# Performance work log

Measured on AMD Instinct MI355X. Metric: run time of the kernel, lower is better.

The kernel has to match this reference:

```python
import jax, jax.numpy as jnp
import numpy as np

# tiny-cuda-nn HashGrid config from the module
N_LEVELS = 12
F_PER_LEVEL = 2
LOG2_T = 16
T = 1 << LOG2_T            # 65536 entries per level
BASE_RES = 4
PER_LEVEL_SCALE = 1.61
HASH_PRIME_Y = np.uint32(2654435761)
HIDDEN = 256
OUT = 3
N_POINTS = 1048576

# per-level scale / resolution (tcnn: scale = base*s^l - 1, res = ceil(scale)+1)
_LEVEL_SCALES = [BASE_RES * (PER_LEVEL_SCALE ** l) - 1.0 for l in range(N_LEVELS)]
_LEVEL_RES = [int(np.ceil(s)) + 1 for s in _LEVEL_SCALES]

_CORNERS = np.array([[0, 0], [1, 0], [0, 1], [1, 1]], dtype=np.uint32)  # [4,2]


def hash_encode(x, tables):
    """x: [N,2] in [0,1); tables: [L,T,F]. Returns [N, L*F]."""
    offs_u = jnp.asarray(_CORNERS)                      # [4,2] uint32
    offs_f = offs_u.astype(x.dtype)                     # [4,2]
    feats = []
    for l in range(N_LEVELS):
        s = _LEVEL_SCALES[l]
        res = _LEVEL_RES[l]
        pos = x * jnp.asarray(s, x.dtype) + 0.5         # [N,2]
        p0f = jnp.floor(pos)
        w = pos - p0f                                   # [N,2] frac, differentiable
        p0 = p0f.astype(jnp.uint32)                     # [N,2]
        c = p0[:, None, :] + offs_u[None]               # [N,4,2] corner coords
        # bilinear weight per corner: prod over dims of (w if offset==1 else 1-w)
        wc = jnp.where(offs_f[None] == 1.0, w[:, None, :], 1.0 - w[:, None, :]).prod(-1)  # [N,4]
        if res * res <= T:
            # dense (tight grid) indexing
            cx = jnp.minimum(c[..., 0], np.uint32(res - 1))
            cy = jnp.minimum(c[..., 1], np.uint32(res - 1))
            idx = cx + cy * np.uint32(res)
        else:
            # spatial hash: x*1 XOR y*prime, masked to table size
            idx = (c[..., 0] ^ (c[..., 1] * HASH_PRIME_Y)) & np.uint32(T - 1)
        f = tables[l][idx.astype(jnp.int32)]            # [N,4,F] gather
        feats.append((wc[..., None] * f).sum(axis=1))   # [N,F]
    return jnp.concatenate(feats, axis=-1)              # [N, L*F]


def setup_inputs() -> dict:
    key = jax.random.key(0)
    ks = jax.random.split(key, 10)
    x = jax.random.uniform(ks[0], (N_POINTS, 2), dtype=jnp.float32)
    # tcnn initializes hash tables uniform in [-1e-4, 1e-4]
    tables = jax.random.uniform(ks[1], (N_LEVELS, T, F_PER_LEVEL), dtype=jnp.float32,
                                minval=-1e-4, maxval=1e-4)
    d_in = N_LEVELS * F_PER_LEVEL

    def lin(k, fan_in, fan_out):
        bound = 1.0 / np.sqrt(fan_in)
        kw, kb = jax.random.split(k)
        W = jax.random.uniform(kw, (fan_in, fan_out), dtype=jnp.float32, minval=-bound, maxval=bound)
        b = jax.random.uniform(kb, (fan_out,), dtype=jnp.float32, minval=-bound, maxval=bound)
        return W, b

    W1, b1 = lin(ks[2], d_in, HIDDEN)
    W2, b2 = lin(ks[3], HIDDEN, HIDDEN)
    W3, b3 = lin(ks[4], HIDDEN, HIDDEN)
    Wo, bo = lin(ks[5], HIDDEN, OUT)
    return {"x": x, "tables": tables, "W1": W1, "b1": b1, "W2": W2, "b2": b2,
            "W3": W3, "b3": b3, "Wo": Wo, "bo": bo}


def reference(x, tables, W1, b1, W2, b2, W3, b3, Wo, bo):
    enc = hash_encode(x, tables)                        # [N,24]
    h = jax.nn.relu(enc @ W1 + b1)
    h = jax.nn.relu(h @ W2 + b2)
    h = jax.nn.relu(h @ W3 + b3)
    return h @ Wo + bo                                  # [N,3]
```

## Files before the change

kernel.cpp:

```cpp
#include <hip/hip_runtime.h>

typedef _Float16 f16;
typedef _Float16 f16x2 __attribute__((ext_vector_type(2)));
typedef _Float16 f16x4 __attribute__((ext_vector_type(4)));
typedef _Float16 f16x8 __attribute__((ext_vector_type(8)));
typedef float    f32x4 __attribute__((ext_vector_type(4)));

#define ES 40
#define NPTS 256

static __device__ const float c_scale[12] = {
  3.0f, 5.44f, 9.3684f, 15.693124f, 25.87592964f, 42.2702467204f,
  68.665097219844f, 111.16080652394884f, 179.5788985035576f,
  289.7320265907278f, 467.0785628110717f, 752.6064861258255f };
static __device__ const unsigned c_res[12] = {4,7,11,17,27,44,70,113,181,291,469,754};

__global__ __launch_bounds__(256) void prep_weights(
    const float* __restrict__ W1, const float* __restrict__ W2,
    const float* __restrict__ W3, const float* __restrict__ Wo,
    f16* __restrict__ ws)
{
  int i = blockIdx.x * 256 + threadIdx.x;
  if (i < 8192) {
    int o = i >> 5, k = i & 31;
    ws[i] = (k < 24) ? (f16)W1[k * 256 + o] : (f16)0.0f;
  } else if (i < 73728) {
    int j = i - 8192; int o = j >> 8, k = j & 255;
    ws[i] = (f16)W2[k * 256 + o];
  } else if (i < 139264) {
    int j = i - 73728; int o = j >> 8, k = j & 255;
    ws[i] = (f16)W3[k * 256 + o];
  } else if (i < 143360) {
    int j = i - 139264; int o = j >> 8, k = j & 255;
    ws[i] = (o < 3) ? (f16)Wo[k * 3 + o] : (f16)0.0f;
  }
}

__device__ __forceinline__ f16x2 enc_level_dense(
    float2 xy, float s, unsigned res, const float* __restrict__ tbl)
{
  float px = __fadd_rn(__fmul_rn(xy.x, s), 0.5f);
  float py = __fadd_rn(__fmul_rn(xy.y, s), 0.5f);
  float fx = floorf(px), fy = floorf(py);
  float wx = px - fx, wy = py - fy;
  unsigned ix = (unsigned)fx, iy = (unsigned)fy;
  unsigned rm = res - 1u;
  unsigned x0 = min(ix, rm);
  unsigned y0 = min(iy, rm), y1 = min(iy + 1u, rm);
  bool xe = (ix >= rm);
  f32x4 r0 = *(const f32x4*)(tbl + (x0 + y0 * res) * 2);
  f32x4 r1 = *(const f32x4*)(tbl + (x0 + y1 * res) * 2);
  float f00x = r0[0], f00y = r0[1];
  float f10x = xe ? r0[0] : r0[2], f10y = xe ? r0[1] : r0[3];
  float f01x = r1[0], f01y = r1[1];
  float f11x = xe ? r1[0] : r1[2], f11y = xe ? r1[1] : r1[3];
  float w00 = (1.f - wx) * (1.f - wy), w10 = wx * (1.f - wy);
  float w01 = (1.f - wx) * wy,         w11 = wx * wy;
  float e0 = w00 * f00x + w10 * f10x + w01 * f01x + w11 * f11x;
  float e1 = w00 * f00y + w10 * f10y + w01 * f01y + w11 * f11y;
  f16x2 pk; pk[0] = (f16)e0; pk[1] = (f16)e1;
  return pk;
}

__device__ __forceinline__ f16x2 enc_level_hash(
    float2 xy, float s, const float* __restrict__ tbl)
{
  float px = __fadd_rn(__fmul_rn(xy.x, s), 0.5f);
  float py = __fadd_rn(__fmul_rn(xy.y, s), 0.5f);
  float fx = floorf(px), fy = floorf(py);
  float wx = px - fx, wy = py - fy;
  unsigned ix = (unsigned)fx, iy = (unsigned)fy;
  unsigned h0 = iy * 2654435761u, h1 = (iy + 1u) * 2654435761u;
  unsigned i00 = (ix ^ h0) & 65535u,  i10 = ((ix + 1u) ^ h0) & 65535u;
  unsigned i01 = (ix ^ h1) & 65535u,  i11 = ((ix + 1u) ^ h1) & 65535u;
  const float2* tb = (const float2*)tbl;
  float2 f00 = tb[i00], f10 = tb[i10], f01 = tb[i01], f11 = tb[i11];
  float w00 = (1.f - wx) * (1.f - wy), w10 = wx * (1.f - wy);
  float w01 = (1.f - wx) * wy,         w11 = wx * wy;
  float e0 = w00 * f00.x + w10 * f10.x + w01 * f01.x + w11 * f11.x;
  float e1 = w00 * f00.y + w10 * f10.y + w01 * f01.y + w11 * f11.y;
  f16x2 pk; pk[0] = (f16)e0; pk[1] = (f16)e1;
  return pk;
}

template<bool NEXT_OUT>
__device__ __forceinline__ void layer256_pipe(
    f16* __restrict__ h, const f16* __restrict__ WT,
    const f32x4* bv, f16x8* cur0, f16x8* cur1,
    const f16* __restrict__ WTn, const float* __restrict__ bn,
    f16x8* nxt0, f16x8* nxt1, f32x4* bvn, f16x8* aout,
    const int* vbase, const int* wbase, int w, int l15, int g)
{
  f32x4 acc[2][16];
  #pragma unroll
  for (int mt = 0; mt < 2; ++mt)
    #pragma unroll
    for (int nt = 0; nt < 16; ++nt) acc[mt][nt] = bv[mt];

  f16x8 abuf[3][2];
  #pragma unroll
  for (int mt = 0; mt < 2; ++mt) { abuf[0][mt] = cur0[mt]; abuf[1][mt] = cur1[mt]; }

  const char* hb = (const char*)h;
  #pragma unroll
  for (int ks = 0; ks < 8; ++ks) {
    if (ks < 6) {
      #pragma unroll
      for (int mt = 0; mt < 2; ++mt)
        abuf[(ks+2)%3][mt] = *(const f16x8*)(WT + (w*32 + mt*16 + l15)*256 + (ks+2)*32 + g*8);
    } else if (ks == 6) {
      if (NEXT_OUT) {
        #pragma unroll
        for (int q = 0; q < 4; ++q)
          aout[q] = *(const f16x8*)(WTn + l15*256 + q*32 + g*8);
      } else {
        #pragma unroll
        for (int mt = 0; mt < 2; ++mt)
          nxt0[mt] = *(const f16x8*)(WTn + (w*32 + mt*16 + l15)*256 + g*8);
        #pragma unroll
        for (int mt = 0; mt < 2; ++mt)
          bvn[mt] = *(const f32x4*)(bn + w*32 + mt*16 + g*4);
      }
    } else {
      if (NEXT_OUT) {
        #pragma unroll
        for (int q = 0; q < 4; ++q)
          aout[4+q] = *(const f16x8*)(WTn + l15*256 + (4+q)*32 + g*8);
      } else {
        #pragma unroll
        for (int mt = 0; mt < 2; ++mt)
          nxt1[mt] = *(const f16x8*)(WTn + (w*32 + mt*16 + l15)*256 + 32 + g*8);
      }
    }
    #pragma unroll
    for (int nt = 0; nt < 16; ++nt) {
      f16x8 b = *(const f16x8*)(hb + vbase[ks] + nt*8192);
      #pragma unroll
      for (int mt = 0; mt < 2; ++mt)
        acc[mt][nt] = __builtin_amdgcn_mfma_f32_16x16x32_f16(abuf[ks%3][mt], b, acc[mt][nt], 0, 0, 0);
    }
  }
  __syncthreads();
  #pragma unroll
  for (int mt = 0; mt < 2; ++mt) {
    #pragma unroll
    for (int nt = 0; nt < 16; ++nt) {
      f16x4 hv;
      #pragma unroll
      for (int r = 0; r < 4; ++r) {
        float v = acc[mt][nt][r];
        hv[r] = (f16)fmaxf(v, 0.0f);
      }
      *(f16x4*)((char*)h + wbase[mt] + nt*8192) = hv;
    }
  }
  __syncthreads();
}

__global__ __launch_bounds__(512, 2) void hashmlp_kernel(
    const float* __restrict__ x, const float* __restrict__ tables,
    const float* __restrict__ b1, const float* __restrict__ b2,
    const float* __restrict__ b3, const float* __restrict__ bo,
    const f16* __restrict__ ws, float* __restrict__ out)
{
  __shared__ __align__(16) f16 s_enc[NPTS * ES];
  __shared__ __align__(16) f16 s_h[NPTS * 256];

  const int tid = threadIdx.x;
  const int blk = blockIdx.x;
  const int w = tid >> 6, lane = tid & 63;
  const int l15 = lane & 15, g = lane >> 4;

  const f16* W1T = ws;
  const f16* W2T = ws + 8192;
  const f16* W3T = ws + 73728;
  const f16* WoT = ws + 139264;

  f16x8 a1[2], pn0[2], pn1[2];
  f32x4 bvA[2], bvB[2];
  #pragma unroll
  for (int mt = 0; mt < 2; ++mt) {
    a1[mt]  = *(const f16x8*)(W1T + (w*32 + mt*16 + l15)*32 + g*8);
    pn0[mt] = *(const f16x8*)(W2T + (w*32 + mt*16 + l15)*256 + g*8);
    pn1[mt] = *(const f16x8*)(W2T + (w*32 + mt*16 + l15)*256 + 32 + g*8);
    bvA[mt] = *(const f32x4*)(b1 + w*32 + mt*16 + g*4);
    bvB[mt] = *(const f32x4*)(b2 + w*32 + mt*16 + g*4);
  }
  float bo0 = bo[0], bo1 = bo[1], bo2 = bo[2];

  int vbase[8], wbase[2];
  {
    int K = (l15 & 7) << 4;
    #pragma unroll
    for (int ks = 0; ks < 8; ++ks)
      vbase[ks] = l15*512 + ((ks*64 + g*16) ^ K);
    #pragma unroll
    for (int mt = 0; mt < 2; ++mt)
      wbase[mt] = l15*512 + (((w*32 + mt*16 + g*4)*2) ^ K);
  }

  {
    int p = tid >> 1, sub = tid & 1;
    int gp = blk * NPTS + p;
    float2 xy = ((const float2*)x)[gp];
    #pragma unroll
    for (int j = 0; j < 5; ++j) {
      int l = j * 2 + sub;
      f16x2 pk = enc_level_dense(xy, c_scale[l], c_res[l], tables + l * 131072);
      *(f16x2*)(&s_enc[p * ES + l * 2]) = pk;
    }
    {
      int l = 10 + sub;
      f16x2 pk = enc_level_hash(xy, c_scale[l], tables + l * 131072);
      *(f16x2*)(&s_enc[p * ES + l * 2]) = pk;
    }
    f16x4 z; z[0] = (f16)0.0f; z[1] = (f16)0.0f; z[2] = (f16)0.0f; z[3] = (f16)0.0f;
    *(f16x4*)(&s_enc[p * ES + 24 + sub * 4]) = z;
  }
  __syncthreads();

  {
    f32x4 acc[2][16];
    #pragma unroll
    for (int mt = 0; mt < 2; ++mt)
      #pragma unroll
      for (int nt = 0; nt < 16; ++nt) acc[mt][nt] = bvA[mt];
    #pragma unroll
    for (int nt = 0; nt < 16; ++nt) {
      f16x8 b = *(const f16x8*)(&s_enc[(nt*16 + l15) * ES + g*8]);
      #pragma unroll
      for (int mt = 0; mt < 2; ++mt)
        acc[mt][nt] = __builtin_amdgcn_mfma_f32_16x16x32_f16(a1[mt], b, acc[mt][nt], 0, 0, 0);
    }
    #pragma unroll
    for (int mt = 0; mt < 2; ++mt) {
      #pragma unroll
      for (int nt = 0; nt < 16; ++nt) {
        f16x4 hv;
        #pragma unroll
        for (int r = 0; r < 4; ++r) {
          float v = acc[mt][nt][r];
          hv[r] = (f16)fmaxf(v, 0.0f);
        }
        *(f16x4*)((char*)s_h + wbase[mt] + nt*8192) = hv;
      }
    }
  }
  __syncthreads();

  f16x8 qn0[2], qn1[2], aout[8];
  f32x4 bvC[2];
  layer256_pipe<false>(s_h, W2T, bvB, pn0, pn1, W3T, b3, qn0, qn1, bvC, aout,
                       vbase, wbase, w, l15, g);
  layer256_pipe<true >(s_h, W3T, bvC, qn0, qn1, WoT, nullptr, pn0, pn1, bvC, aout,
                       vbase, wbase, w, l15, g);

  {
    f32x4 acc0 = (f32x4)0.0f, acc1 = (f32x4)0.0f;
    const char* hb = (const char*)s_h;
    #pragma unroll
    for (int ks = 0; ks < 8; ++ks) {
      f16x8 b0 = *(const f16x8*)(hb + vbase[ks] + (2*w+0)*8192);
      f16x8 b1v = *(const f16x8*)(hb + vbase[ks] + (2*w+1)*8192);
      acc0 = __builtin_amdgcn_mfma_f32_16x16x32_f16(aout[ks], b0, acc0, 0, 0, 0);
      acc1 = __builtin_amdgcn_mfma_f32_16x16x32_f16(aout[ks], b1v, acc1, 0, 0, 0);
    }
    if (g == 0) {
      int gp0 = blk * NPTS + (2*w+0) * 16 + l15;
      int gp1 = blk * NPTS + (2*w+1) * 16 + l15;
      out[gp0 * 3 + 0] = acc0[0] + bo0;
      out[gp0 * 3 + 1] = acc0[1] + bo1;
      out[gp0 * 3 + 2] = acc0[2] + bo2;
      out[gp1 * 3 + 0] = acc1[0] + bo0;
      out[gp1 * 3 + 1] = acc1[1] + bo1;
      out[gp1 * 3 + 2] = acc1[2] + bo2;
    }
  }
}

extern "C" void kernel_launch(void* const* d_in, const int* in_sizes, int n_in,
                              void* d_out, int out_size, void* d_ws, size_t ws_size,
                              hipStream_t stream) {
  const float* x  = (const float*)d_in[0];
  const float* tb = (const float*)d_in[1];
  const float* W1 = (const float*)d_in[2];
  const float* b1 = (const float*)d_in[3];
  const float* W2 = (const float*)d_in[4];
  const float* b2 = (const float*)d_in[5];
  const float* W3 = (const float*)d_in[6];
  const float* b3 = (const float*)d_in[7];
  const float* Wo = (const float*)d_in[8];
  const float* bo = (const float*)d_in[9];
  f16* ws = (f16*)d_ws;

  prep_weights<<<560, 256, 0, stream>>>(W1, W2, W3, Wo, ws);
  hashmlp_kernel<<<4096, 512, 0, stream>>>(x, tb, b1, b2, b3, bo, ws, (float*)d_out);
}
```

Measured before the change: 363.8 us.

## Switch MLP layers to 32x32x16 MFMA tiles with 128-point, 4-wave blocks

Replaces the 16x16x32 MFMA tiling of the hidden layers with 32x32x16 MFMA, giving each wave 64 output neurons by 128 points. The block shrinks from 256 points and 8 waves to 128 points and 4 waves, and the grid doubles. The larger MFMA tile is meant to raise operand reuse per LDS read and cut the number of LDS B-fragment loads. In exchange it uses more accumulator registers per wave, adds more weight fragment loads per wave, and needs new swizzled address tables; the encoding step and the output layer keep their previous structure.

```diff
diff --git a/kernel.cpp b/kernel.cpp
--- a/kernel.cpp
+++ b/kernel.cpp
@@ -4,10 +4,11 @@
 typedef _Float16 f16x2 __attribute__((ext_vector_type(2)));
 typedef _Float16 f16x4 __attribute__((ext_vector_type(4)));
 typedef _Float16 f16x8 __attribute__((ext_vector_type(8)));
-typedef float    f32x4 __attribute__((ext_vector_type(4)));
+typedef float    f32x4  __attribute__((ext_vector_type(4)));
+typedef float    f32x16 __attribute__((ext_vector_type(16)));
 
 #define ES 40
-#define NPTS 256
+#define NPTS 128
 
 static __device__ const float c_scale[12] = {
   3.0f, 5.44f, 9.3684f, 15.693124f, 25.87592964f, 42.2702467204f,
@@ -84,18 +85,26 @@
 }
 
 template<bool NEXT_OUT>
-__device__ __forceinline__ void layer256_pipe(
+__device__ __forceinline__ void layer256_32(
     f16* __restrict__ h, const f16* __restrict__ WT,
-    const f32x4* bv, f16x8* cur0, f16x8* cur1,
+    const f32x4 (&bv)[2][4], f16x8* cur0, f16x8* cur1,
     const f16* __restrict__ WTn, const float* __restrict__ bn,
-    f16x8* nxt0, f16x8* nxt1, f32x4* bvn, f16x8* aout,
-    const int* vbase, const int* wbase, int w, int l15, int g)
-{
-  f32x4 acc[2][16];
+    f16x8* nxt0, f16x8* nxt1, f32x4 (*bvn)[4], f16x8* aout,
+    const int* vbase, const int (&wb)[2][4],
+    int w, int l31, int g2, int l15, int g)
+{
+  f32x16 acc[2][4];
   #pragma unroll
   for (int mt = 0; mt < 2; ++mt)
     #pragma unroll
-    for (int nt = 0; nt < 16; ++nt) acc[mt][nt] = bv[mt];
+    for (int rq = 0; rq < 4; ++rq) {
+      f32x4 t = bv[mt][rq];
+      #pragma unroll
+      for (int nt = 0; nt < 4; ++nt)
+        #pragma unroll
+        for (int j = 0; j < 4; ++j)
+          acc[mt][nt][rq*4+j] = t[j];
+    }
 
   f16x8 abuf[3][2];
   #pragma unroll
@@ -103,12 +112,12 @@
 
   const char* hb = (const char*)h;
   #pragma unroll
-  for (int ks = 0; ks < 8; ++ks) {
-    if (ks < 6) {
+  for (int ks = 0; ks < 16; ++ks) {
+    if (ks < 14) {
       #pragma unroll
       for (int mt = 0; mt < 2; ++mt)
-        abuf[(ks+2)%3][mt] = *(const f16x8*)(WT + (w*32 + mt*16 + l15)*256 + (ks+2)*32 + g*8);
-    } else if (ks == 6) {
+        abuf[(ks+2)%3][mt] = *(const f16x8*)(WT + (w*64 + mt*32 + l31)*256 + (ks+2)*16 + g2*8);
+    } else if (ks == 14) {
       if (NEXT_OUT) {
         #pragma unroll
         for (int q = 0; q < 4; ++q)
@@ -116,10 +125,12 @@
       } else {
         #pragma unroll
         for (int mt = 0; mt < 2; ++mt)
-          nxt0[mt] = *(const f16x8*)(WTn + (w*32 + mt*16 + l15)*256 + g*8);
+          nxt0[mt] = *(const f16x8*)(WTn + (w*64 + mt*32 + l31)*256 + g2*8);
         #pragma unroll
         for (int mt = 0; mt < 2; ++mt)
-          bvn[mt] = *(const f32x4*)(bn + w*32 + mt*16 + g*4);
+          #pragma unroll
+          for (int rq = 0; rq < 4; ++rq)
+            bvn[mt][rq] = *(const f32x4*)(bn + w*64 + mt*32 + rq*8 + g2*4);
       }
     } else {
       if (NEXT_OUT) {
@@ -129,35 +140,34 @@
       } else {
         #pragma unroll
         for (int mt = 0; mt < 2; ++mt)
-          nxt1[mt] = *(const f16x8*)(WTn + (w*32 + mt*16 + l15)*256 + 32 + g*8);
-      }
-    }
-    #pragma unroll
-    for (int nt = 0; nt < 16; ++nt) {
-      f16x8 b = *(const f16x8*)(hb + vbase[ks] + nt*8192);
+          nxt1[mt] = *(const f16x8*)(WTn + (w*64 + mt*32 + l31)*256 + 16 + g2*8);
+      }
+    }
+    #pragma unroll
+    for (int nt = 0; nt < 4; ++nt) {
+      f16x8 b = *(const f16x8*)(hb + vbase[ks] + nt*16384);
       #pragma unroll
       for (int mt = 0; mt < 2; ++mt)
-        acc[mt][nt] = __builtin_amdgcn_mfma_f32_16x16x32_f16(abuf[ks%3][mt], b, acc[mt][nt], 0, 0, 0);
+        acc[mt][nt] = __builtin_amdgcn_mfma_f32_32x32x16_f16(abuf[ks%3][mt], b, acc[mt][nt], 0, 0, 0);
     }
   }
   __syncthreads();
   #pragma unroll
-  for (int mt = 0; mt < 2; ++mt) {
-    #pragma unroll
-    for (int nt = 0; nt < 16; ++nt) {
-      f16x4 hv;
-      #pragma unroll
-      for (int r = 0; r < 4; ++r) {
-        float v = acc[mt][nt][r];
-        hv[r] = (f16)fmaxf(v, 0.0f);
-      }
-      *(f16x4*)((char*)h + wbase[mt] + nt*8192) = hv;
-    }
-  }
+  for (int mt = 0; mt < 2; ++mt)
+    #pragma unroll
+    for (int nt = 0; nt < 4; ++nt)
+      #pragma unroll
+      for (int rq = 0; rq < 4; ++rq) {
+        f16x4 hv;
+        #pragma unroll
+        for (int j = 0; j < 4; ++j)
+          hv[j] = (f16)fmaxf(acc[mt][nt][rq*4+j], 0.0f);
+        *(f16x4*)((char*)h + wb[mt][rq] + nt*16384) = hv;
+      }
   __syncthreads();
 }
 
-__global__ __launch_bounds__(512, 2) void hashmlp_kernel(
+__global__ __launch_bounds__(256, 2) void hashmlp_kernel(
     const float* __restrict__ x, const float* __restrict__ tables,
     const float* __restrict__ b1, const float* __restrict__ b2,
     const float* __restrict__ b3, const float* __restrict__ bo,
@@ -169,6 +179,7 @@
   const int tid = threadIdx.x;
   const int blk = blockIdx.x;
   const int w = tid >> 6, lane = tid & 63;
+  const int l31 = lane & 31, g2 = lane >> 5;
   const int l15 = lane & 15, g = lane >> 4;
 
   const f16* W1T = ws;
@@ -176,27 +187,35 @@
   const f16* W3T = ws + 73728;
   const f16* WoT = ws + 139264;
 
-  f16x8 a1[2], pn0[2], pn1[2];
-  f32x4 bvA[2], bvB[2];
+  f16x8 a1[2][2], pn0[2], pn1[2];
+  f32x4 bvA[2][4], bvB[2][4];
   #pragma unroll
   for (int mt = 0; mt < 2; ++mt) {
-    a1[mt]  = *(const f16x8*)(W1T + (w*32 + mt*16 + l15)*32 + g*8);
-    pn0[mt] = *(const f16x8*)(W2T + (w*32 + mt*16 + l15)*256 + g*8);
-    pn1[mt] = *(const f16x8*)(W2T + (w*32 + mt*16 + l15)*256 + 32 + g*8);
-    bvA[mt] = *(const f32x4*)(b1 + w*32 + mt*16 + g*4);
-    bvB[mt] = *(const f32x4*)(b2 + w*32 + mt*16 + g*4);
+    #pragma unroll
+    for (int ks = 0; ks < 2; ++ks)
+      a1[ks][mt] = *(const f16x8*)(W1T + (w*64 + mt*32 + l31)*32 + ks*16 + g2*8);
+    pn0[mt] = *(const f16x8*)(W2T + (w*64 + mt*32 + l31)*256 + g2*8);
+    pn1[mt] = *(const f16x8*)(W2T + (w*64 + mt*32 + l31)*256 + 16 + g2*8);
+    #pragma unroll
+    for (int rq = 0; rq < 4; ++rq) {
+      bvA[mt][rq] = *(const f32x4*)(b1 + w*64 + mt*32 + rq*8 + g2*4);
+      bvB[mt][rq] = *(const f32x4*)(b2 + w*64 + mt*32 + rq*8 + g2*4);
+    }
   }
   float bo0 = bo[0], bo1 = bo[1], bo2 = bo[2];
 
-  int vbase[8], wbase[2];
+  int vbase[16];
+  int wb[2][4];
   {
-    int K = (l15 & 7) << 4;
-    #pragma unroll
-    for (int ks = 0; ks < 8; ++ks)
-      vbase[ks] = l15*512 + ((ks*64 + g*16) ^ K);
+    int K = (l31 & 7) << 4;
+    #pragma unroll
+    for (int ks = 0; ks < 16; ++ks)
+      vbase[ks] = l31*512 + ((ks*32 + g2*16) ^ K);
     #pragma unroll
     for (int mt = 0; mt < 2; ++mt)
-      wbase[mt] = l15*512 + (((w*32 + mt*16 + g*4)*2) ^ K);
+      #pragma unroll
+      for (int rq = 0; rq < 4; ++rq)
+        wb[mt][rq] = l31*512 + (((w*64 + mt*32 + rq*8 + g2*4) * 2) ^ K);
   }
 
   {
@@ -220,48 +239,58 @@
   __syncthreads();
 
   {
-    f32x4 acc[2][16];
+    f32x16 acc[2][4];
     #pragma unroll
     for (int mt = 0; mt < 2; ++mt)
       #pragma unroll
-      for (int nt = 0; nt < 16; ++nt) acc[mt][nt] = bvA[mt];
-    #pragma unroll
-    for (int nt = 0; nt < 16; ++nt) {
-      f16x8 b = *(const f16x8*)(&s_enc[(nt*16 + l15) * ES + g*8]);
-      #pragma unroll
-      for (int mt = 0; mt < 2; ++mt)
-        acc[mt][nt] = __builtin_amdgcn_mfma_f32_16x16x32_f16(a1[mt], b, acc[mt][nt], 0, 0, 0);
-    }
-    #pragma unroll
-    for (int mt = 0; mt < 2; ++mt) {
-      #pragma unroll
-      for (int nt = 0; nt < 16; ++nt) {
-        f16x4 hv;
-        #pragma unroll
-        for (int r = 0; r < 4; ++r) {
-          float v = acc[mt][nt][r];
-          hv[r] = (f16)fmaxf(v, 0.0f);
+      for (int rq = 0; rq < 4; ++rq) {
+        f32x4 t = bvA[mt][rq];
+        #pragma unroll
+        for (int nt = 0; nt < 4; ++nt)
+          #pragma unroll
+          for (int j = 0; j < 4; ++j)
+            acc[mt][nt][rq*4+j] = t[j];
+      }
+    #pragma unroll
+    for (int ks = 0; ks < 2; ++ks)
+      #pragma unroll
+      for (int nt = 0; nt < 4; ++nt) {
+        f16x8 b = *(const f16x8*)(&s_enc[(nt*32 + l31) * ES + ks*16 + g2*8]);
+        #pragma unroll
+        for (int mt = 0; mt < 2; ++mt)
+          acc[mt][nt] = __builtin_amdgcn_mfma_f32_32x32x16_f16(a1[ks][mt], b, acc[mt][nt], 0, 0, 0);
+      }
+    #pragma unroll
+    for (int mt = 0; mt < 2; ++mt)
+      #pragma unroll
+      for (int nt = 0; nt < 4; ++nt)
+        #pragma unroll
+        for (int rq = 0; rq < 4; ++rq) {
+          f16x4 hv;
+          #pragma unroll
+          for (int j = 0; j < 4; ++j)
+            hv[j] = (f16)fmaxf(acc[mt][nt][rq*4+j], 0.0f);
+          *(f16x4*)((char*)s_h + wb[mt][rq] + nt*16384) = hv;
         }
-        *(f16x4*)((char*)s_h + wbase[mt] + nt*8192) = hv;
-      }
-    }
   }
   __syncthreads();
 
   f16x8 qn0[2], qn1[2], aout[8];
-  f32x4 bvC[2];
-  layer256_pipe<false>(s_h, W2T, bvB, pn0, pn1, W3T, b3, qn0, qn1, bvC, aout,
-                       vbase, wbase, w, l15, g);
-  layer256_pipe<true >(s_h, W3T, bvC, qn0, qn1, WoT, nullptr, pn0, pn1, bvC, aout,
-                       vbase, wbase, w, l15, g);
+  f32x4 bvC[2][4];
+  layer256_32<false>(s_h, W2T, bvB, pn0, pn1, W3T, b3, qn0, qn1, bvC, aout,
+                     vbase, wb, w, l31, g2, l15, g);
+  layer256_32<true >(s_h, W3T, bvC, qn0, qn1, WoT, nullptr, pn0, pn1, bvC, aout,
+                     vbase, wb, w, l31, g2, l15, g);
 
   {
+    const int K16 = (l15 & 7) << 4;
     f32x4 acc0 = (f32x4)0.0f, acc1 = (f32x4)0.0f;
     const char* hb = (const char*)s_h;
     #pragma unroll
     for (int ks = 0; ks < 8; ++ks) {
-      f16x8 b0 = *(const f16x8*)(hb + vbase[ks] + (2*w+0)*8192);
-      f16x8 b1v = *(const f16x8*)(hb + vbase[ks] + (2*w+1)*8192);
+      int off = l15*512 + ((ks*64 + g*16) ^ K16);
+      f16x8 b0 = *(const f16x8*)(hb + off + (2*w+0)*8192);
+      f16x8 b1v = *(const f16x8*)(hb + off + (2*w+1)*8192);
       acc0 = __builtin_amdgcn_mfma_f32_16x16x32_f16(aout[ks], b0, acc0, 0, 0, 0);
       acc1 = __builtin_amdgcn_mfma_f32_16x16x32_f16(aout[ks], b1v, acc1, 0, 0, 0);
     }
@@ -294,5 +323,5 @@
   f16* ws = (f16*)d_ws;
 
   prep_weights<<<560, 256, 0, stream>>>(W1, W2, W3, Wo, ws);
-  hashmlp_kernel<<<4096, 512, 0, stream>>>(x, tb, b1, b2, b3, bo, ws, (float*)d_out);
-}
+  hashmlp_kernel<<<8192, 256, 0, stream>>>(x, tb, b1, b2, b3, bo, ws, (float*)d_out);
+}
```

Result: no change. 363.9 us (+0.0%).
